# Kernel optimization log

Measured on AMD Instinct MI355X. Metric: run time of the kernel, lower is better.

Reference implementation:

```python
import jax, jax.numpy as jnp
import numpy as np

DIM = 1024
HEADS = 16
HEAD_DIM = DIM // HEADS
SCALE = HEAD_DIM ** -0.5


def setup_inputs() -> dict:
    key = jax.random.key(0)
    k1, k2, k3, k4 = jax.random.split(key, 4)
    x = jax.random.normal(k1, (2, 2048, DIM), dtype=jnp.float32)
    # nn.Linear(dim, 3*dim, bias=False): weight shape (3*dim, dim), y = x @ W.T
    w_qkv = jax.random.normal(k2, (3 * DIM, DIM), dtype=jnp.float32) * (DIM ** -0.5)
    w_proj = jax.random.normal(k3, (DIM, DIM), dtype=jnp.float32) * (DIM ** -0.5)
    head_w = jnp.ones((HEADS,), dtype=jnp.float32)
    return {"x": x, "w_qkv": w_qkv, "w_proj": w_proj, "head_w": head_w}


def reference(x, w_qkv, w_proj, head_w) -> jnp.ndarray:
    B, N, C = x.shape
    qkv = jnp.einsum("bnc,dc->bnd", x, w_qkv)  # [B,N,3C]
    qkv = qkv.reshape(B, N, 3, HEADS, HEAD_DIM).transpose(2, 0, 3, 1, 4)
    q, k, v = qkv[0], qkv[1], qkv[2]  # each [B,H,N,Dh]
    attn = jnp.einsum("bhqd,bhkd->bhqk", q, k) * SCALE  # [B,H,N,N]
    attn = jax.nn.softmax(attn, axis=-1)
    out = jnp.einsum("bhqk,bhkd->bhqd", attn, v)  # [B,H,N,Dh]
    hw = jax.nn.softmax(head_w)[None, :, None, None]
    out = out * hw
    out = out.transpose(0, 2, 1, 3).reshape(B, N, C)
    return jnp.einsum("bnc,dc->bnd", out, w_proj)
```

## Files before the change

### kernel.cpp

```cpp
#include <hip/hip_runtime.h>

typedef _Float16 half_t;
typedef _Float16 half8 __attribute__((ext_vector_type(8)));
typedef _Float16 half4_t __attribute__((ext_vector_type(4)));
typedef float floatx4 __attribute__((ext_vector_type(4)));

#define B_SZ 2
#define SEQ 2048
#define DIM_ 1024
#define NH 16
#define DH 64
#define ROWS (B_SZ * SEQ)

__device__ __forceinline__ void gl2lds16(const void* g, void* l) {
  __builtin_amdgcn_global_load_lds((const __attribute__((address_space(1))) unsigned int*)g,
                                   (__attribute__((address_space(3))) unsigned int*)l, 16, 0, 0);
}

__global__ void convert_all(const float4* __restrict__ x, const float4* __restrict__ wq,
                            const float4* __restrict__ wp, half4_t* __restrict__ dst,
                            int nx, int nq, int np) {
  int i = blockIdx.x * blockDim.x + threadIdx.x;
  float4 v;
  if (i < nx) v = x[i];
  else if (i < nx + nq) v = wq[i - nx];
  else if (i < nx + nq + np) v = wp[i - nx - nq];
  else return;
  half4_t h;
  h.x = (half_t)v.x; h.y = (half_t)v.y; h.z = (half_t)v.z; h.w = (half_t)v.w;
  dst[i] = h;
}

template <int MODE>
__global__ __launch_bounds__(256) void gemm128(const half_t* __restrict__ A,
                                               const half_t* __restrict__ Bt,
                                               half_t* __restrict__ q16,
                                               half_t* __restrict__ k16,
                                               half_t* __restrict__ vT16,
                                               float* __restrict__ outp) {
  constexpr int K = 1024;
  __shared__ __align__(16) half_t a_lds[128 * 32];
  __shared__ __align__(16) half_t b_lds[128 * 32];
  const int t = threadIdx.x;
  const int wave = t >> 6, lane = t & 63;
  const int l15 = lane & 15, quad = lane >> 4;
  const int wm = wave >> 1, wn = wave & 1;
  const int row0 = blockIdx.y * 128, col0 = blockIdx.x * 128;

  floatx4 acc[4][4];
  const floatx4 z4 = {0.f, 0.f, 0.f, 0.f};
#pragma unroll
  for (int i = 0; i < 4; ++i)
#pragma unroll
    for (int j = 0; j < 4; ++j) acc[i][j] = z4;

  for (int k0 = 0; k0 < K; k0 += 32) {
#pragma unroll
    for (int hi = 0; hi < 2; ++hi) {
      int s = t + hi * 256;
      int row = s >> 2, c = s & 3;
      int sc = c ^ ((row >> 1) & 3);
      gl2lds16(A + (size_t)(row0 + row) * K + (k0 + sc * 8), a_lds + (wave * 64 + hi * 256) * 8);
      gl2lds16(Bt + (size_t)(col0 + row) * K + (k0 + sc * 8), b_lds + (wave * 64 + hi * 256) * 8);
    }
    __syncthreads();
    half8 af[4], bf[4];
#pragma unroll
    for (int mt = 0; mt < 4; ++mt) {
      int row = wm * 64 + mt * 16 + l15;
      af[mt] = *(const half8*)(a_lds + row * 32 + (quad ^ ((row >> 1) & 3)) * 8);
    }
#pragma unroll
    for (int nt = 0; nt < 4; ++nt) {
      int row = wn * 64 + nt * 16 + l15;
      bf[nt] = *(const half8*)(b_lds + row * 32 + (quad ^ ((row >> 1) & 3)) * 8);
    }
#pragma unroll
    for (int mt = 0; mt < 4; ++mt)
#pragma unroll
      for (int nt = 0; nt < 4; ++nt)
        acc[mt][nt] = __builtin_amdgcn_mfma_f32_16x16x32_f16(af[mt], bf[nt], acc[mt][nt], 0, 0, 0);
    __syncthreads();
  }

  if (MODE == 0) {
    const int which = col0 >> 10;
#pragma unroll
    for (int mt = 0; mt < 4; ++mt)
#pragma unroll
      for (int nt = 0; nt < 4; ++nt) {
        int rbase = row0 + wm * 64 + mt * 16 + quad * 4;
        int gcol = col0 + wn * 64 + nt * 16 + l15;
        int hc = gcol & 1023, h = hc >> 6, d = hc & 63;
        int b = rbase >> 11, n0 = rbase & 2047;
        int bh = b * NH + h;
        if (which == 2) {
          half4_t h4;
          h4.x = (half_t)acc[mt][nt][0];
          h4.y = (half_t)acc[mt][nt][1];
          h4.z = (half_t)acc[mt][nt][2];
          h4.w = (half_t)acc[mt][nt][3];
          *(half4_t*)(vT16 + ((size_t)bh * DH + d) * SEQ + n0) = h4;
        } else {
#pragma unroll
          for (int r = 0; r < 4; ++r) {
            float v = acc[mt][nt][r];
            if (which == 0)
              q16[((size_t)bh * SEQ + n0 + r) * DH + d] = (half_t)(v * 0.125f);
            else
              k16[((size_t)bh * SEQ + n0 + r) * DH + d] = (half_t)v;
          }
        }
      }
  } else {
#pragma unroll
    for (int mt = 0; mt < 4; ++mt)
#pragma unroll
      for (int nt = 0; nt < 4; ++nt) {
        int rbase = row0 + wm * 64 + mt * 16 + quad * 4;
        int gcol = col0 + wn * 64 + nt * 16 + l15;
#pragma unroll
        for (int r = 0; r < 4; ++r)
          outp[(size_t)(rbase + r) * DIM_ + gcol] = acc[mt][nt][r];
      }
  }
}

__global__ __launch_bounds__(256) void attn_fa(const half_t* __restrict__ q16,
                                               const half_t* __restrict__ k16,
                                               const half_t* __restrict__ vT16,
                                               const float* __restrict__ head_w,
                                               half_t* __restrict__ attn16) {
  __shared__ __align__(16) half_t k_lds[2][64 * 64];
  __shared__ __align__(16) half_t v_lds[2][64 * 64];
  __shared__ __align__(16) half_t p_lds[8 * 1024];

  const int t = threadIdx.x;
  const int wave = t >> 6, lane = t & 63;
  const int l15 = lane & 15, quad = lane >> 4;
  const int bh = blockIdx.x >> 4, qt = blockIdx.x & 15;
  const int h = bh & 15, b = bh >> 4;
  const half_t* qp = q16 + (size_t)bh * SEQ * DH;
  const half_t* kp = k16 + (size_t)bh * SEQ * DH;
  const half_t* vp = vT16 + (size_t)bh * DH * SEQ;
  const int q0w = qt * 128 + wave * 32;

  const int s0 = t, s1 = t + 256;
  const int r0_ = s0 >> 3, c0_ = (s0 & 7) ^ (r0_ & 7);
  const int r1_ = s1 >> 3, c1_ = (s1 & 7) ^ (r1_ & 7);

  half8 qf[2][2];
#pragma unroll
  for (int mi = 0; mi < 2; ++mi)
#pragma unroll
    for (int kf = 0; kf < 2; ++kf)
      qf[mi][kf] = *(const half8*)(qp + (size_t)(q0w + mi * 16 + l15) * DH + kf * 32 + quad * 8);

  const floatx4 z4 = {0.f, 0.f, 0.f, 0.f};
  floatx4 o[2][4];
  float psum[2][4];
#pragma unroll
  for (int mi = 0; mi < 2; ++mi)
#pragma unroll
    for (int i = 0; i < 4; ++i) { o[mi][i] = z4; psum[mi][i] = 0.f; }

  const int prow = quad * 4;
  const int rswz = (l15 + (l15 >> 3)) & 7;

  gl2lds16(kp + (size_t)r0_ * DH + c0_ * 8, &k_lds[0][(wave * 64) * 8]);
  gl2lds16(vp + (size_t)r0_ * SEQ + c0_ * 8, &v_lds[0][(wave * 64) * 8]);
  gl2lds16(kp + (size_t)r1_ * DH + c1_ * 8, &k_lds[0][(wave * 64 + 256) * 8]);
  gl2lds16(vp + (size_t)r1_ * SEQ + c1_ * 8, &v_lds[0][(wave * 64 + 256) * 8]);

  int cur = 0;
  for (int jt = 0; jt < 32; ++jt) {
    __syncthreads();

    if (jt + 1 < 32) {
      const int j0 = (jt + 1) * 64, nb = cur ^ 1;
      gl2lds16(kp + (size_t)(j0 + r0_) * DH + c0_ * 8, &k_lds[nb][(wave * 64) * 8]);
      gl2lds16(vp + (size_t)r0_ * SEQ + j0 + c0_ * 8, &v_lds[nb][(wave * 64) * 8]);
      gl2lds16(kp + (size_t)(j0 + r1_) * DH + c1_ * 8, &k_lds[nb][(wave * 64 + 256) * 8]);
      gl2lds16(vp + (size_t)r1_ * SEQ + j0 + c1_ * 8, &v_lds[nb][(wave * 64 + 256) * 8]);
    }

    const half_t* kl = k_lds[cur];
    const half_t* vl = v_lds[cur];

    floatx4 sacc[2][4];
#pragma unroll
    for (int mi = 0; mi < 2; ++mi)
#pragma unroll
      for (int nt = 0; nt < 4; ++nt) sacc[mi][nt] = z4;
#pragma unroll
    for (int kf = 0; kf < 2; ++kf)
#pragma unroll
      for (int nt = 0; nt < 4; ++nt) {
        int row = nt * 16 + l15;
        half8 kb = *(const half8*)(kl + row * 64 + (((kf << 2) | quad) ^ (row & 7)) * 8);
        sacc[0][nt] = __builtin_amdgcn_mfma_f32_16x16x32_f16(qf[0][kf], kb, sacc[0][nt], 0, 0, 0);
        sacc[1][nt] = __builtin_amdgcn_mfma_f32_16x16x32_f16(qf[1][kf], kb, sacc[1][nt], 0, 0, 0);
      }

#pragma unroll
    for (int mi = 0; mi < 2; ++mi) {
      half_t* pw = p_lds + (wave * 2 + mi) * 1024;
#pragma unroll
      for (int nt = 0; nt < 4; ++nt)
#pragma unroll
        for (int r = 0; r < 4; ++r) {
          float p = __expf(sacc[mi][nt][r]);
          psum[mi][r] += p;
          int row = prow + r, col = nt * 16 + l15;
          int swz = (row + (row >> 3)) & 7;
          pw[row * 64 + (((col >> 3) ^ swz) << 3) + (col & 7)] = (half_t)p;
        }
    }

#pragma unroll
    for (int kf = 0; kf < 2; ++kf) {
      half8 pf0 = *(const half8*)(p_lds + (wave * 2 + 0) * 1024 + l15 * 64 +
                                  ((((kf << 2) | quad) ^ rswz) << 3));
      half8 pf1 = *(const half8*)(p_lds + (wave * 2 + 1) * 1024 + l15 * 64 +
                                  ((((kf << 2) | quad) ^ rswz) << 3));
#pragma unroll
      for (int nt = 0; nt < 4; ++nt) {
        int vrow = nt * 16 + l15;
        half8 vb = *(const half8*)(vl + vrow * 64 + (((kf << 2) | quad) ^ (vrow & 7)) * 8);
        o[0][nt] = __builtin_amdgcn_mfma_f32_16x16x32_f16(pf0, vb, o[0][nt], 0, 0, 0);
        o[1][nt] = __builtin_amdgcn_mfma_f32_16x16x32_f16(pf1, vb, o[1][nt], 0, 0, 0);
      }
    }
    cur ^= 1;
  }

#pragma unroll
  for (int mi = 0; mi < 2; ++mi)
#pragma unroll
    for (int r = 0; r < 4; ++r) {
#pragma unroll
      for (int dm = 1; dm < 16; dm <<= 1) psum[mi][r] += __shfl_xor(psum[mi][r], dm, 64);
    }

  float mw = head_w[0];
#pragma unroll
  for (int i = 1; i < NH; ++i) mw = fmaxf(mw, head_w[i]);
  float sw = 0.f;
#pragma unroll
  for (int i = 0; i < NH; ++i) sw += __expf(head_w[i] - mw);
  float hwv = __expf(head_w[h] - mw) / sw;

#pragma unroll
  for (int mi = 0; mi < 2; ++mi)
#pragma unroll
    for (int r = 0; r < 4; ++r) {
      float scl = hwv / psum[mi][r];
      int n = q0w + mi * 16 + quad * 4 + r;
#pragma unroll
      for (int nt = 0; nt < 4; ++nt) {
        int col = h * DH + nt * 16 + l15;
        attn16[((size_t)(b * SEQ + n)) * DIM_ + col] = (half_t)(o[mi][nt][r] * scl);
      }
    }
}

extern "C" void kernel_launch(void* const* d_in, const int* in_sizes, int n_in,
                              void* d_out, int out_size, void* d_ws, size_t ws_size,
                              hipStream_t stream) {
  const float* x = (const float*)d_in[0];
  const float* w_qkv = (const float*)d_in[1];
  const float* w_proj = (const float*)d_in[2];
  const float* head_w = (const float*)d_in[3];
  float* out = (float*)d_out;

  half_t* x16 = (half_t*)d_ws;
  half_t* wq16 = x16 + (size_t)ROWS * DIM_;
  half_t* wp16 = wq16 + (size_t)3 * DIM_ * DIM_;
  half_t* q16 = wp16 + (size_t)DIM_ * DIM_;
  half_t* k16 = q16 + (size_t)ROWS * DIM_;
  half_t* vT16 = k16 + (size_t)ROWS * DIM_;
  half_t* attn16 = vT16 + (size_t)ROWS * DIM_;

  const int nx = ROWS * DIM_ / 4, nq = 3 * DIM_ * DIM_ / 4, np = DIM_ * DIM_ / 4;
  convert_all<<<(nx + nq + np) / 256, 256, 0, stream>>>((const float4*)x, (const float4*)w_qkv,
                                                        (const float4*)w_proj, (half4_t*)x16,
                                                        nx, nq, np);

  gemm128<0><<<dim3(24, 32), 256, 0, stream>>>(x16, wq16, q16, k16, vT16, nullptr);
  attn_fa<<<B_SZ * NH * (SEQ / 128), 256, 0, stream>>>(q16, k16, vT16, head_w, attn16);
  gemm128<1><<<dim3(8, 32), 256, 0, stream>>>(attn16, wp16, nullptr, nullptr, nullptr, out);
}
```

Baseline: 207.4 us.

## Keep attention probabilities in registers via transposed S and retile projection GEMM

```diff
diff --git a/kernel.cpp b/kernel.cpp
--- a/kernel.cpp
+++ b/kernel.cpp
@@ -31,7 +31,7 @@
   dst[i] = h;
 }
 
-template <int MODE>
+template <int MODE, int BN>
 __global__ __launch_bounds__(256) void gemm128(const half_t* __restrict__ A,
                                                const half_t* __restrict__ Bt,
                                                half_t* __restrict__ q16,
@@ -39,20 +39,21 @@
                                                half_t* __restrict__ vT16,
                                                float* __restrict__ outp) {
   constexpr int K = 1024;
+  constexpr int NT = BN / 32;
   __shared__ __align__(16) half_t a_lds[128 * 32];
-  __shared__ __align__(16) half_t b_lds[128 * 32];
+  __shared__ __align__(16) half_t b_lds[BN * 32];
   const int t = threadIdx.x;
   const int wave = t >> 6, lane = t & 63;
   const int l15 = lane & 15, quad = lane >> 4;
   const int wm = wave >> 1, wn = wave & 1;
-  const int row0 = blockIdx.y * 128, col0 = blockIdx.x * 128;
-
-  floatx4 acc[4][4];
+  const int row0 = blockIdx.y * 128, col0 = blockIdx.x * BN;
+
+  floatx4 acc[4][NT];
   const floatx4 z4 = {0.f, 0.f, 0.f, 0.f};
 #pragma unroll
   for (int i = 0; i < 4; ++i)
 #pragma unroll
-    for (int j = 0; j < 4; ++j) acc[i][j] = z4;
+    for (int j = 0; j < NT; ++j) acc[i][j] = z4;
 
   for (int k0 = 0; k0 < K; k0 += 32) {
 #pragma unroll
@@ -61,24 +62,30 @@
       int row = s >> 2, c = s & 3;
       int sc = c ^ ((row >> 1) & 3);
       gl2lds16(A + (size_t)(row0 + row) * K + (k0 + sc * 8), a_lds + (wave * 64 + hi * 256) * 8);
+    }
+#pragma unroll
+    for (int hi = 0; hi < BN / 64; ++hi) {
+      int s = t + hi * 256;
+      int row = s >> 2, c = s & 3;
+      int sc = c ^ ((row >> 1) & 3);
       gl2lds16(Bt + (size_t)(col0 + row) * K + (k0 + sc * 8), b_lds + (wave * 64 + hi * 256) * 8);
     }
     __syncthreads();
-    half8 af[4], bf[4];
+    half8 af[4], bf[NT];
 #pragma unroll
     for (int mt = 0; mt < 4; ++mt) {
       int row = wm * 64 + mt * 16 + l15;
       af[mt] = *(const half8*)(a_lds + row * 32 + (quad ^ ((row >> 1) & 3)) * 8);
     }
 #pragma unroll
-    for (int nt = 0; nt < 4; ++nt) {
-      int row = wn * 64 + nt * 16 + l15;
+    for (int nt = 0; nt < NT; ++nt) {
+      int row = wn * NT * 16 + nt * 16 + l15;
       bf[nt] = *(const half8*)(b_lds + row * 32 + (quad ^ ((row >> 1) & 3)) * 8);
     }
 #pragma unroll
     for (int mt = 0; mt < 4; ++mt)
 #pragma unroll
-      for (int nt = 0; nt < 4; ++nt)
+      for (int nt = 0; nt < NT; ++nt)
         acc[mt][nt] = __builtin_amdgcn_mfma_f32_16x16x32_f16(af[mt], bf[nt], acc[mt][nt], 0, 0, 0);
     __syncthreads();
   }
@@ -88,9 +95,9 @@
 #pragma unroll
     for (int mt = 0; mt < 4; ++mt)
 #pragma unroll
-      for (int nt = 0; nt < 4; ++nt) {
+      for (int nt = 0; nt < NT; ++nt) {
         int rbase = row0 + wm * 64 + mt * 16 + quad * 4;
-        int gcol = col0 + wn * 64 + nt * 16 + l15;
+        int gcol = col0 + wn * NT * 16 + nt * 16 + l15;
         int hc = gcol & 1023, h = hc >> 6, d = hc & 63;
         int b = rbase >> 11, n0 = rbase & 2047;
         int bh = b * NH + h;
@@ -116,9 +123,9 @@
 #pragma unroll
     for (int mt = 0; mt < 4; ++mt)
 #pragma unroll
-      for (int nt = 0; nt < 4; ++nt) {
+      for (int nt = 0; nt < NT; ++nt) {
         int rbase = row0 + wm * 64 + mt * 16 + quad * 4;
-        int gcol = col0 + wn * 64 + nt * 16 + l15;
+        int gcol = col0 + wn * NT * 16 + nt * 16 + l15;
 #pragma unroll
         for (int r = 0; r < 4; ++r)
           outp[(size_t)(rbase + r) * DIM_ + gcol] = acc[mt][nt][r];
@@ -133,7 +140,6 @@
                                                half_t* __restrict__ attn16) {
   __shared__ __align__(16) half_t k_lds[2][64 * 64];
   __shared__ __align__(16) half_t v_lds[2][64 * 64];
-  __shared__ __align__(16) half_t p_lds[8 * 1024];
 
   const int t = threadIdx.x;
   const int wave = t >> 6, lane = t & 63;
@@ -158,14 +164,11 @@
 
   const floatx4 z4 = {0.f, 0.f, 0.f, 0.f};
   floatx4 o[2][4];
-  float psum[2][4];
+  float psum[2] = {0.f, 0.f};
 #pragma unroll
   for (int mi = 0; mi < 2; ++mi)
 #pragma unroll
-    for (int i = 0; i < 4; ++i) { o[mi][i] = z4; psum[mi][i] = 0.f; }
-
-  const int prow = quad * 4;
-  const int rswz = (l15 + (l15 >> 3)) & 7;
+    for (int i = 0; i < 4; ++i) o[mi][i] = z4;
 
   gl2lds16(kp + (size_t)r0_ * DH + c0_ * 8, &k_lds[0][(wave * 64) * 8]);
   gl2lds16(vp + (size_t)r0_ * SEQ + c0_ * 8, &v_lds[0][(wave * 64) * 8]);
@@ -187,60 +190,54 @@
     const half_t* kl = k_lds[cur];
     const half_t* vl = v_lds[cur];
 
-    floatx4 sacc[2][4];
+    floatx4 st[2][4];
 #pragma unroll
     for (int mi = 0; mi < 2; ++mi)
 #pragma unroll
-      for (int nt = 0; nt < 4; ++nt) sacc[mi][nt] = z4;
+      for (int nt = 0; nt < 4; ++nt) st[mi][nt] = z4;
 #pragma unroll
     for (int kf = 0; kf < 2; ++kf)
 #pragma unroll
       for (int nt = 0; nt < 4; ++nt) {
         int row = nt * 16 + l15;
         half8 kb = *(const half8*)(kl + row * 64 + (((kf << 2) | quad) ^ (row & 7)) * 8);
-        sacc[0][nt] = __builtin_amdgcn_mfma_f32_16x16x32_f16(qf[0][kf], kb, sacc[0][nt], 0, 0, 0);
-        sacc[1][nt] = __builtin_amdgcn_mfma_f32_16x16x32_f16(qf[1][kf], kb, sacc[1][nt], 0, 0, 0);
-      }
-
-#pragma unroll
-    for (int mi = 0; mi < 2; ++mi) {
-      half_t* pw = p_lds + (wave * 2 + mi) * 1024;
-#pragma unroll
-      for (int nt = 0; nt < 4; ++nt)
-#pragma unroll
-        for (int r = 0; r < 4; ++r) {
-          float p = __expf(sacc[mi][nt][r]);
-          psum[mi][r] += p;
-          int row = prow + r, col = nt * 16 + l15;
-          int swz = (row + (row >> 3)) & 7;
-          pw[row * 64 + (((col >> 3) ^ swz) << 3) + (col & 7)] = (half_t)p;
-        }
-    }
-
-#pragma unroll
-    for (int kf = 0; kf < 2; ++kf) {
-      half8 pf0 = *(const half8*)(p_lds + (wave * 2 + 0) * 1024 + l15 * 64 +
-                                  ((((kf << 2) | quad) ^ rswz) << 3));
-      half8 pf1 = *(const half8*)(p_lds + (wave * 2 + 1) * 1024 + l15 * 64 +
-                                  ((((kf << 2) | quad) ^ rswz) << 3));
+        st[0][nt] = __builtin_amdgcn_mfma_f32_16x16x32_f16(kb, qf[0][kf], st[0][nt], 0, 0, 0);
+        st[1][nt] = __builtin_amdgcn_mfma_f32_16x16x32_f16(kb, qf[1][kf], st[1][nt], 0, 0, 0);
+      }
+
+    half4_t pf[2][4];
+#pragma unroll
+    for (int mi = 0; mi < 2; ++mi)
 #pragma unroll
       for (int nt = 0; nt < 4; ++nt) {
-        int vrow = nt * 16 + l15;
-        half8 vb = *(const half8*)(vl + vrow * 64 + (((kf << 2) | quad) ^ (vrow & 7)) * 8);
-        o[0][nt] = __builtin_amdgcn_mfma_f32_16x16x32_f16(pf0, vb, o[0][nt], 0, 0, 0);
-        o[1][nt] = __builtin_amdgcn_mfma_f32_16x16x32_f16(pf1, vb, o[1][nt], 0, 0, 0);
-      }
-    }
+        float p0 = __expf(st[mi][nt][0]);
+        float p1 = __expf(st[mi][nt][1]);
+        float p2 = __expf(st[mi][nt][2]);
+        float p3 = __expf(st[mi][nt][3]);
+        psum[mi] += (p0 + p1) + (p2 + p3);
+        half4_t pk;
+        pk.x = (half_t)p0; pk.y = (half_t)p1; pk.z = (half_t)p2; pk.w = (half_t)p3;
+        pf[mi][nt] = pk;
+      }
+
+#pragma unroll
+    for (int jt2 = 0; jt2 < 4; ++jt2)
+#pragma unroll
+      for (int dt = 0; dt < 4; ++dt) {
+        int row = dt * 16 + l15;
+        int ch = (jt2 * 2 + (quad >> 1)) ^ (l15 & 7);
+        half4_t vb = *(const half4_t*)(vl + row * 64 + ch * 8 + (quad & 1) * 4);
+        o[0][dt] = __builtin_amdgcn_mfma_f32_16x16x16f16(pf[0][jt2], vb, o[0][dt], 0, 0, 0);
+        o[1][dt] = __builtin_amdgcn_mfma_f32_16x16x16f16(pf[1][jt2], vb, o[1][dt], 0, 0, 0);
+      }
     cur ^= 1;
   }
 
 #pragma unroll
-  for (int mi = 0; mi < 2; ++mi)
-#pragma unroll
-    for (int r = 0; r < 4; ++r) {
-#pragma unroll
-      for (int dm = 1; dm < 16; dm <<= 1) psum[mi][r] += __shfl_xor(psum[mi][r], dm, 64);
-    }
+  for (int mi = 0; mi < 2; ++mi) {
+    psum[mi] += __shfl_xor(psum[mi], 16, 64);
+    psum[mi] += __shfl_xor(psum[mi], 32, 64);
+  }
 
   float mw = head_w[0];
 #pragma unroll
@@ -254,12 +251,13 @@
   for (int mi = 0; mi < 2; ++mi)
 #pragma unroll
     for (int r = 0; r < 4; ++r) {
-      float scl = hwv / psum[mi][r];
+      float ps = __shfl(psum[mi], quad * 4 + r, 64);
+      float scl = hwv / ps;
       int n = q0w + mi * 16 + quad * 4 + r;
 #pragma unroll
-      for (int nt = 0; nt < 4; ++nt) {
-        int col = h * DH + nt * 16 + l15;
-        attn16[((size_t)(b * SEQ + n)) * DIM_ + col] = (half_t)(o[mi][nt][r] * scl);
+      for (int dt = 0; dt < 4; ++dt) {
+        int col = h * DH + dt * 16 + l15;
+        attn16[((size_t)(b * SEQ + n)) * DIM_ + col] = (half_t)(o[mi][dt][r] * scl);
       }
     }
 }
@@ -286,7 +284,7 @@
                                                         (const float4*)w_proj, (half4_t*)x16,
                                                         nx, nq, np);
 
-  gemm128<0><<<dim3(24, 32), 256, 0, stream>>>(x16, wq16, q16, k16, vT16, nullptr);
+  gemm128<0, 128><<<dim3(24, 32), 256, 0, stream>>>(x16, wq16, q16, k16, vT16, nullptr);
   attn_fa<<<B_SZ * NH * (SEQ / 128), 256, 0, stream>>>(q16, k16, vT16, head_w, attn16);
-  gemm128<1><<<dim3(8, 32), 256, 0, stream>>>(attn16, wp16, nullptr, nullptr, nullptr, out);
-}
+  gemm128<1, 64><<<dim3(16, 32), 256, 0, stream>>>(attn16, wp16, nullptr, nullptr, nullptr, out);
+}
```

Result: faster. 202.9 us (-2.2%).
